# Kernel optimization log

Hardware: AMD Instinct MI355X
Metric: run time of the kernel (lower is better)

Reference implementation:

```python
import jax, jax.numpy as jnp
import numpy as np

B = 8192      # number of molecules (graphs)
T = 524288    # total flat candidates (avg 64 per graph, jagged)
D = 128       # embed_dim
V = 100000    # unique templates (table has V+1 rows incl. 'unknown')


def setup_inputs() -> dict:
    key = jax.random.key(0)
    k1, k2, k3 = jax.random.split(key, 3)
    rng = np.random.default_rng(0)
    # jagged lengths, each segment >= 1, summing exactly to T
    lengths = rng.multinomial(T - B, np.ones(B) / B) + 1
    seg_ids = np.repeat(np.arange(B), lengths)           # [T], sorted segment ids
    offsets = np.concatenate([[0], np.cumsum(lengths)[:-1]])
    target_pos = offsets + rng.integers(0, lengths)      # one target per segment
    return {
        "graph_embed": jax.random.normal(k1, (B, D), dtype=jnp.float32),
        "tpl_embedding": jax.random.normal(k2, (V + 1, D), dtype=jnp.float32),
        "cand_idx": jax.random.randint(k3, (T,), 0, V + 1),
        "seg_ids": jnp.asarray(seg_ids, dtype=jnp.int32),
        "target_pos": jnp.asarray(target_pos, dtype=jnp.int32),
    }


def reference(graph_embed, tpl_embedding, cand_idx, seg_ids, target_pos):
    num_seg = graph_embed.shape[0]
    # gather candidate (template) embeddings: [T, D]
    cand_embed = tpl_embedding[cand_idx]
    # gather graph embedding per candidate (torch.gather with rep_indices): [T, D]
    g = graph_embed[seg_ids]
    # inner-product attention score per candidate: [T]
    logits = jnp.sum(g * cand_embed, axis=1)
    # jagged (segment-wise) log-softmax over variable-length candidate lists
    seg_max = jax.ops.segment_max(logits, seg_ids, num_segments=num_seg)
    shifted = logits - seg_max[seg_ids]
    seg_sum = jax.ops.segment_sum(jnp.exp(shifted), seg_ids, num_segments=num_seg)
    log_prob = shifted - jnp.log(seg_sum)[seg_ids]
    # gather the log-prob of the target template per graph: [B]
    return log_prob[target_pos]
```

## Files before the change

### kernel.cpp

```cpp
#include <hip/hip_runtime.h>

#define D 128
#define LOG2E 1.4426950408889634f
#define LN2   0.6931471805599453f

__global__ void seg_bounds_kernel(const int* __restrict__ seg_ids,
                                  int* __restrict__ seg_start,
                                  int T, int B) {
    int t = blockIdx.x * blockDim.x + threadIdx.x;
    if (t >= T) return;
    if (t == 0) {
        seg_start[0] = 0;
    } else if (seg_ids[t] != seg_ids[t - 1]) {
        seg_start[seg_ids[t]] = t;
    }
    if (t == T - 1) seg_start[B] = T;
}

__global__ __launch_bounds__(256) void logits_kernel(
    const float* __restrict__ graph_embed,
    const float* __restrict__ tpl_embedding,
    const int* __restrict__ cand_idx,
    const int* __restrict__ seg_ids,
    float* __restrict__ logits,
    int T)
{
    const int sl  = threadIdx.x & 31;
    const int hw  = (blockIdx.x * blockDim.x + threadIdx.x) >> 5;
    const int nhw = (gridDim.x * blockDim.x) >> 5;

    for (int t0 = hw; t0 < T; t0 += 2 * nhw) {
        const int t1 = t0 + nhw;
        const bool has1 = (t1 < T);

        const int c0 = cand_idx[t0];
        const int s0 = seg_ids[t0];
        const int c1 = has1 ? cand_idx[t1] : c0;
        const int s1 = has1 ? seg_ids[t1] : s0;

        const float4 x0 = ((const float4*)(tpl_embedding + (size_t)c0 * D))[sl];
        const float4 g0 = ((const float4*)(graph_embed   + (size_t)s0 * D))[sl];
        const float4 x1 = ((const float4*)(tpl_embedding + (size_t)c1 * D))[sl];
        const float4 g1 = ((const float4*)(graph_embed   + (size_t)s1 * D))[sl];

        float p0 = fmaf(g0.x, x0.x, fmaf(g0.y, x0.y, fmaf(g0.z, x0.z, g0.w * x0.w)));
        float p1 = fmaf(g1.x, x1.x, fmaf(g1.y, x1.y, fmaf(g1.z, x1.z, g1.w * x1.w)));

        #pragma unroll
        for (int off = 16; off >= 1; off >>= 1) {
            p0 += __shfl_xor(p0, off);
            p1 += __shfl_xor(p1, off);
        }
        if (sl == 0) {
            logits[t0] = p0;
            if (has1) logits[t1] = p1;
        }
    }
}

__global__ __launch_bounds__(64) void seg_reduce_kernel(
    const float* __restrict__ logits,
    const int* __restrict__ seg_start,
    const int* __restrict__ target_pos,
    float* __restrict__ out)
{
    const int b    = blockIdx.x;
    const int lane = threadIdx.x;
    const int start = seg_start[b];
    const int end   = seg_start[b + 1];

    float m = -3.0e38f;
    float s = 0.0f;

    for (int t = start + lane; t < end; t += 64) {
        const float x = logits[t] * LOG2E;
        if (x <= m) {
            s += exp2f(x - m);
        } else {
            s = fmaf(s, exp2f(m - x), 1.0f);
            m = x;
        }
    }

    #pragma unroll
    for (int off = 32; off >= 1; off >>= 1) {
        const float m2 = __shfl_xor(m, off);
        const float s2 = __shfl_xor(s, off);
        const float M  = fmaxf(m, m2);
        s = s * exp2f(m - M) + s2 * exp2f(m2 - M);
        m = M;
    }

    if (lane == 0) {
        const float tl = logits[target_pos[b]] * LOG2E;
        out[b] = (tl - m - log2f(s)) * LN2;
    }
}

extern "C" void kernel_launch(void* const* d_in, const int* in_sizes, int n_in,
                              void* d_out, int out_size, void* d_ws, size_t ws_size,
                              hipStream_t stream) {
    const float* graph_embed   = (const float*)d_in[0];
    const float* tpl_embedding = (const float*)d_in[1];
    const int*   cand_idx      = (const int*)d_in[2];
    const int*   seg_ids       = (const int*)d_in[3];
    const int*   target_pos    = (const int*)d_in[4];
    float*       out           = (float*)d_out;

    const int B = in_sizes[0] / D;
    const int T = in_sizes[2];

    int*   seg_start = (int*)d_ws;
    float* logits    = (float*)d_ws + (((B + 1) + 63) & ~63);

    seg_bounds_kernel<<<(T + 255) / 256, 256, 0, stream>>>(seg_ids, seg_start, T, B);

    logits_kernel<<<2048, 256, 0, stream>>>(graph_embed, tpl_embedding,
                                            cand_idx, seg_ids, logits, T);

    seg_reduce_kernel<<<B, 64, 0, stream>>>(logits, seg_start, target_pos, out);
}
```

Baseline: 134.9 us.

## Bucket candidates by template index range to improve gather locality

Adds a per-call counting sort that buckets candidates into 64 ranges of template index (2048 rows each) via a block histogram, a scan and a scatter kernel, producing a permutation. The logits kernel then processes candidates in bucketed order, so concurrent waves gather nearby embedding-table rows and should hit cache more often. In exchange it adds three extra kernels plus a memset, an extra indirection per candidate, and scattered logit writes and graph_embed reads. The old path is kept as a fallback when the workspace is too small.

```diff
diff --git a/kernel.cpp b/kernel.cpp
--- a/kernel.cpp
+++ b/kernel.cpp
@@ -3,59 +3,199 @@
 #define D 128
 #define LOG2E 1.4426950408889634f
 #define LN2   0.6931471805599453f
+#define BINS   64
+#define BSHIFT 11
+
+
+__global__ __launch_bounds__(256) void count_bounds_kernel(
+    const int* __restrict__ cand_idx,
+    const int* __restrict__ seg_ids,
+    int* __restrict__ block_counts,
+    int* __restrict__ totals,
+    int* __restrict__ seg_start,
+    int T, int B, int nblk)
+{
+    __shared__ int h[BINS];
+    const int tid = threadIdx.x;
+    if (tid < BINS) h[tid] = 0;
+    __syncthreads();
+
+    const int base = blockIdx.x * 1024 + tid * 4;
+    #pragma unroll
+    for (int j = 0; j < 4; ++j) {
+        const int i = base + j;
+        if (i < T) atomicAdd(&h[cand_idx[i] >> BSHIFT], 1);
+    }
+    #pragma unroll
+    for (int j = 0; j < 4; ++j) {
+        const int i = base + j;
+        if (i < T) {
+            if (i == 0) seg_start[0] = 0;
+            else if (seg_ids[i] != seg_ids[i - 1]) seg_start[seg_ids[i]] = i;
+            if (i == T - 1) seg_start[B] = T;
+        }
+    }
+    __syncthreads();
+    if (tid < BINS) {
+        block_counts[tid * nblk + blockIdx.x] = h[tid];
+        atomicAdd(&totals[tid], h[tid]);
+    }
+}
+
+__global__ __launch_bounds__(64) void binscan_kernel(
+    const int* __restrict__ block_counts,
+    const int* __restrict__ totals,
+    int* __restrict__ block_base,
+    int nblk)
+{
+    const int k    = blockIdx.x;
+    const int lane = threadIdx.x;
+
+    int t = (lane < k) ? totals[lane] : 0;
+    #pragma unroll
+    for (int off = 32; off >= 1; off >>= 1) t += __shfl_xor(t, off);
+    const int bin_start = t;
+
+    const int base = lane * 8;
+    int vals[8];
+    int s = 0;
+    #pragma unroll
+    for (int j = 0; j < 8; ++j) {
+        const int b = base + j;
+        vals[j] = (b < nblk) ? block_counts[k * nblk + b] : 0;
+        s += vals[j];
+    }
+    int inc = s;
+    #pragma unroll
+    for (int off = 1; off < 64; off <<= 1) {
+        const int up = __shfl_up(inc, off);
+        if (lane >= off) inc += up;
+    }
+    int run = bin_start + (inc - s);
+    #pragma unroll
+    for (int j = 0; j < 8; ++j) {
+        const int b = base + j;
+        if (b < nblk) block_base[k * nblk + b] = run;
+        run += vals[j];
+    }
+}
+
+__global__ __launch_bounds__(256) void scatter_kernel(
+    const int* __restrict__ cand_idx,
+    const int* __restrict__ block_base,
+    int* __restrict__ perm,
+    int T, int nblk)
+{
+    __shared__ int h[BINS];
+    const int tid = threadIdx.x;
+    if (tid < BINS) h[tid] = 0;
+    __syncthreads();
+
+    const int base = blockIdx.x * 1024 + tid * 4;
+    #pragma unroll
+    for (int j = 0; j < 4; ++j) {
+        const int i = base + j;
+        if (i < T) {
+            const int bkt = cand_idx[i] >> BSHIFT;
+            const int r   = atomicAdd(&h[bkt], 1);
+            perm[block_base[bkt * nblk + blockIdx.x] + r] = i;
+        }
+    }
+}
+
+__global__ __launch_bounds__(256) void logits_perm_kernel(
+    const float* __restrict__ graph_embed,
+    const float* __restrict__ tpl_embedding,
+    const int* __restrict__ cand_idx,
+    const int* __restrict__ seg_ids,
+    const int* __restrict__ perm,
+    float* __restrict__ logits,
+    int T)
+{
+    const int sl  = threadIdx.x & 31;
+    const int hw  = (blockIdx.x * blockDim.x + threadIdx.x) >> 5;
+    const int nhw = (gridDim.x * blockDim.x) >> 5;
+
+    for (int i0 = hw; i0 < T; i0 += 2 * nhw) {
+        const int i1   = i0 + nhw;
+        const bool has1 = (i1 < T);
+
+        const int t0 = perm[i0];
+        const int t1 = has1 ? perm[i1] : t0;
+
+        const int c0 = cand_idx[t0];
+        const int s0 = seg_ids[t0];
+        const int c1 = cand_idx[t1];
+        const int s1 = seg_ids[t1];
+
+        const float4 x0 = ((const float4*)(tpl_embedding + (size_t)c0 * D))[sl];
+        const float4 g0 = ((const float4*)(graph_embed   + (size_t)s0 * D))[sl];
+        const float4 x1 = ((const float4*)(tpl_embedding + (size_t)c1 * D))[sl];
+        const float4 g1 = ((const float4*)(graph_embed   + (size_t)s1 * D))[sl];
+
+        float p0 = fmaf(g0.x, x0.x, fmaf(g0.y, x0.y, fmaf(g0.z, x0.z, g0.w * x0.w)));
+        float p1 = fmaf(g1.x, x1.x, fmaf(g1.y, x1.y, fmaf(g1.z, x1.z, g1.w * x1.w)));
+
+        #pragma unroll
+        for (int off = 16; off >= 1; off >>= 1) {
+            p0 += __shfl_xor(p0, off);
+            p1 += __shfl_xor(p1, off);
+        }
+        if (sl == 0) {
+            logits[t0] = p0;
+            if (has1) logits[t1] = p1;
+        }
+    }
+}
+
+__global__ __launch_bounds__(256) void logits_kernel(
+    const float* __restrict__ graph_embed,
+    const float* __restrict__ tpl_embedding,
+    const int* __restrict__ cand_idx,
+    const int* __restrict__ seg_ids,
+    float* __restrict__ logits,
+    int T)
+{
+    const int sl  = threadIdx.x & 31;
+    const int hw  = (blockIdx.x * blockDim.x + threadIdx.x) >> 5;
+    const int nhw = (gridDim.x * blockDim.x) >> 5;
+
+    for (int t0 = hw; t0 < T; t0 += 2 * nhw) {
+        const int t1 = t0 + nhw;
+        const bool has1 = (t1 < T);
+        const int c0 = cand_idx[t0];
+        const int s0 = seg_ids[t0];
+        const int c1 = has1 ? cand_idx[t1] : c0;
+        const int s1 = has1 ? seg_ids[t1] : s0;
+
+        const float4 x0 = ((const float4*)(tpl_embedding + (size_t)c0 * D))[sl];
+        const float4 g0 = ((const float4*)(graph_embed   + (size_t)s0 * D))[sl];
+        const float4 x1 = ((const float4*)(tpl_embedding + (size_t)c1 * D))[sl];
+        const float4 g1 = ((const float4*)(graph_embed   + (size_t)s1 * D))[sl];
+
+        float p0 = fmaf(g0.x, x0.x, fmaf(g0.y, x0.y, fmaf(g0.z, x0.z, g0.w * x0.w)));
+        float p1 = fmaf(g1.x, x1.x, fmaf(g1.y, x1.y, fmaf(g1.z, x1.z, g1.w * x1.w)));
+
+        #pragma unroll
+        for (int off = 16; off >= 1; off >>= 1) {
+            p0 += __shfl_xor(p0, off);
+            p1 += __shfl_xor(p1, off);
+        }
+        if (sl == 0) {
+            logits[t0] = p0;
+            if (has1) logits[t1] = p1;
+        }
+    }
+}
 
 __global__ void seg_bounds_kernel(const int* __restrict__ seg_ids,
                                   int* __restrict__ seg_start,
                                   int T, int B) {
     int t = blockIdx.x * blockDim.x + threadIdx.x;
     if (t >= T) return;
-    if (t == 0) {
-        seg_start[0] = 0;
-    } else if (seg_ids[t] != seg_ids[t - 1]) {
-        seg_start[seg_ids[t]] = t;
-    }
+    if (t == 0) seg_start[0] = 0;
+    else if (seg_ids[t] != seg_ids[t - 1]) seg_start[seg_ids[t]] = t;
     if (t == T - 1) seg_start[B] = T;
-}
-
-__global__ __launch_bounds__(256) void logits_kernel(
-    const float* __restrict__ graph_embed,
-    const float* __restrict__ tpl_embedding,
-    const int* __restrict__ cand_idx,
-    const int* __restrict__ seg_ids,
-    float* __restrict__ logits,
-    int T)
-{
-    const int sl  = threadIdx.x & 31;
-    const int hw  = (blockIdx.x * blockDim.x + threadIdx.x) >> 5;
-    const int nhw = (gridDim.x * blockDim.x) >> 5;
-
-    for (int t0 = hw; t0 < T; t0 += 2 * nhw) {
-        const int t1 = t0 + nhw;
-        const bool has1 = (t1 < T);
-
-        const int c0 = cand_idx[t0];
-        const int s0 = seg_ids[t0];
-        const int c1 = has1 ? cand_idx[t1] : c0;
-        const int s1 = has1 ? seg_ids[t1] : s0;
-
-        const float4 x0 = ((const float4*)(tpl_embedding + (size_t)c0 * D))[sl];
-        const float4 g0 = ((const float4*)(graph_embed   + (size_t)s0 * D))[sl];
-        const float4 x1 = ((const float4*)(tpl_embedding + (size_t)c1 * D))[sl];
-        const float4 g1 = ((const float4*)(graph_embed   + (size_t)s1 * D))[sl];
-
-        float p0 = fmaf(g0.x, x0.x, fmaf(g0.y, x0.y, fmaf(g0.z, x0.z, g0.w * x0.w)));
-        float p1 = fmaf(g1.x, x1.x, fmaf(g1.y, x1.y, fmaf(g1.z, x1.z, g1.w * x1.w)));
-
-        #pragma unroll
-        for (int off = 16; off >= 1; off >>= 1) {
-            p0 += __shfl_xor(p0, off);
-            p1 += __shfl_xor(p1, off);
-        }
-        if (sl == 0) {
-            logits[t0] = p0;
-            if (has1) logits[t1] = p1;
-        }
-    }
 }
 
 __global__ __launch_bounds__(64) void seg_reduce_kernel(
@@ -109,14 +249,39 @@
 
     const int B = in_sizes[0] / D;
     const int T = in_sizes[2];
-
-    int*   seg_start = (int*)d_ws;
-    float* logits    = (float*)d_ws + (((B + 1) + 63) & ~63);
-
-    seg_bounds_kernel<<<(T + 255) / 256, 256, 0, stream>>>(seg_ids, seg_start, T, B);
-
-    logits_kernel<<<2048, 256, 0, stream>>>(graph_embed, tpl_embedding,
-                                            cand_idx, seg_ids, logits, T);
+    const int nblk = (T + 1023) / 1024;
+
+    size_t off = 0;
+    auto alloc = [&](size_t bytes) {
+        void* p = (char*)d_ws + off;
+        off += (bytes + 255) & ~(size_t)255;
+        return p;
+    };
+    int*   seg_start    = (int*)  alloc((size_t)(B + 1) * 4);
+    float* logits       = (float*)alloc((size_t)T * 4);
+    int*   perm         = (int*)  alloc((size_t)T * 4);
+    int*   block_counts = (int*)  alloc((size_t)BINS * nblk * 4);
+    int*   block_base   = (int*)  alloc((size_t)BINS * nblk * 4);
+    int*   totals       = (int*)  alloc((size_t)BINS * 4);
+
+    const bool bucketed = (off <= ws_size) && (nblk <= 512);
+
+    if (bucketed) {
+        hipMemsetAsync(totals, 0, BINS * 4, stream);
+        count_bounds_kernel<<<nblk, 256, 0, stream>>>(cand_idx, seg_ids,
+                                                      block_counts, totals,
+                                                      seg_start, T, B, nblk);
+        binscan_kernel<<<BINS, 64, 0, stream>>>(block_counts, totals,
+                                                block_base, nblk);
+        scatter_kernel<<<nblk, 256, 0, stream>>>(cand_idx, block_base, perm, T, nblk);
+        logits_perm_kernel<<<2048, 256, 0, stream>>>(graph_embed, tpl_embedding,
+                                                     cand_idx, seg_ids, perm,
+                                                     logits, T);
+    } else {
+        seg_bounds_kernel<<<(T + 255) / 256, 256, 0, stream>>>(seg_ids, seg_start, T, B);
+        logits_kernel<<<2048, 256, 0, stream>>>(graph_embed, tpl_embedding,
+                                                cand_idx, seg_ids, logits, T);
+    }
 
     seg_reduce_kernel<<<B, 64, 0, stream>>>(logits, seg_start, target_pos, out);
 }
```

After: 179.8 us. +33.2%, slower.
